# Kernel tuning notes

Hardware: AMD Instinct MI355X
Metric: run time of the kernel (lower is better)

The kernel has to match this reference:

```python
import jax, jax.numpy as jnp
import numpy as np

B, L, T = 32, 100, 50
V_SENT, V_FIELD, V_POS = 20000, 1500, 31
E_S, E_F, E_P = 400, 50, 5
FREP = E_F + 2 * E_P            # field rep = field + ppos + pneg embeds
H_DEC = 500                      # decoder hidden
H_DIR = H_DEC // 2               # per-direction encoder hidden
H_ENC = 500                      # encoder_hidden_size (attention/output dim)
IN_ENC = E_S + FREP
EPS = 1e-3


def lstm_cell(x, h, c, Wih, Whh, b):
    z = x @ Wih.T + h @ Whh.T + b
    i, f, g, o = jnp.split(z, 4, axis=-1)
    c = jax.nn.sigmoid(f) * c + jax.nn.sigmoid(i) * jnp.tanh(g)
    h = jax.nn.sigmoid(o) * jnp.tanh(c)
    return h, c


def setup_inputs():
    key = jax.random.key(0)
    ks = jax.random.split(key, 30)
    n = lambda k, sh, s=0.05: jax.random.normal(k, sh, jnp.float32) * s
    return {
        "value_mask": jnp.ones((B, L), jnp.float32),
        "align_prob": jax.random.uniform(ks[0], (B, L, V_SENT), jnp.float32),
        "E_sent": n(ks[1], (V_SENT, E_S)),
        "E_field": n(ks[2], (V_FIELD, E_F)),
        "E_ppos": n(ks[3], (V_POS, E_P)),
        "E_pneg": n(ks[4], (V_POS, E_P)),
        "E_target": n(ks[5], (V_SENT, 300)),
        "enc_Wih_f": n(ks[6], (4 * H_DIR, IN_ENC)),
        "enc_Whh_f": n(ks[7], (4 * H_DIR, H_DIR)),
        "enc_b_f": jnp.zeros((4 * H_DIR,), jnp.float32),
        "enc_Wih_b": n(ks[8], (4 * H_DIR, IN_ENC)),
        "enc_Whh_b": n(ks[9], (4 * H_DIR, H_DIR)),
        "enc_b_b": jnp.zeros((4 * H_DIR,), jnp.float32),
        "dec_Wih": n(ks[10], (4 * H_DEC, E_S)),
        "dec_Whh": n(ks[11], (4 * H_DEC, H_DEC)),
        "dec_b": jnp.zeros((4 * H_DEC,), jnp.float32),
        "W_d": n(ks[12], (H_DEC, H_ENC)),
        "W_z": n(ks[13], (H_DEC, FREP)),
        "W_out": n(ks[14], (H_DEC + H_ENC, H_ENC)),
        "b_out": jnp.zeros((H_ENC,), jnp.float32),
        "w_l": n(ks[15], (H_DEC + H_ENC + E_S, 1)),
        "b_l": jnp.zeros((1,), jnp.float32),
        "W_lin": n(ks[16], (V_SENT, H_ENC)),
        "b_lin": jnp.zeros((V_SENT,), jnp.float32),
        "sent": jax.random.randint(ks[17], (B, T), 0, V_SENT),
        "value": jax.random.randint(ks[18], (B, L), 0, V_SENT),
        "field": jax.random.randint(ks[19], (B, L), 0, V_FIELD),
        "ppos": jax.random.randint(ks[20], (B, L), 0, V_POS),
        "pneg": jax.random.randint(ks[21], (B, L), 0, V_POS),
        "batch_size": B,
    }


def _forward(value_mask, align_prob, E_sent, E_field, E_ppos, E_pneg, E_target,
             enc_Wih_f, enc_Whh_f, enc_b_f, enc_Wih_b, enc_Whh_b, enc_b_b,
             dec_Wih, dec_Whh, dec_b, W_d, W_z, W_out, b_out, w_l, b_l,
             W_lin, b_lin, sent, value, field, ppos, pneg):
    bsz = value.shape[0]
    inp_d = E_sent[value]                                             # [B,L,E_S]
    inp_z = jnp.concatenate([E_field[field], E_ppos[ppos], E_pneg[pneg]], axis=-1)  # [B,L,FREP]
    x = jnp.concatenate([inp_d, inp_z], axis=-1)                      # [B,L,IN_ENC]
    xs = jnp.transpose(x, (1, 0, 2))                                  # [L,B,IN_ENC]
    h0 = jnp.zeros((bsz, H_DIR), x.dtype)

    def enc_step(Wih, Whh, b):
        def f(carry, xt):
            h, c = lstm_cell(xt, carry[0], carry[1], Wih, Whh, b)
            return (h, c), h
        return f

    (hf, cf), hs_f = jax.lax.scan(enc_step(enc_Wih_f, enc_Whh_f, enc_b_f), (h0, h0), xs)
    (hb, cb), hs_b = jax.lax.scan(enc_step(enc_Wih_b, enc_Whh_b, enc_b_b), (h0, h0), xs[::-1])
    enc_out = jnp.transpose(jnp.concatenate([hs_f, hs_b[::-1]], axis=-1), (1, 0, 2))  # [B,L,H_ENC]
    # replicate torch .view on h_n [2,B,H_DIR] -> [B, 2*H_DIR] (row-major, as in source)
    h0_dec = jnp.stack([hf, hb]).reshape(bsz, 2 * H_DIR)
    c0_dec = jnp.stack([cf, cb]).reshape(bsz, 2 * H_DIR)

    sent_emb = jnp.transpose(E_sent[sent], (1, 0, 2))                 # [T,B,E_S]

    def dec_step(carry, xt):
        h, c = lstm_cell(xt, carry[0], carry[1], dec_Wih, dec_Whh, dec_b)
        s_d = jnp.einsum('be,ble->bl', h @ W_d, enc_out)              # attn over encoder states
        s_z = jnp.einsum('bf,blf->bl', h @ W_z, inp_z)                # attn over field reps
        a = jax.nn.softmax(s_d, axis=-1) * jax.nn.softmax(s_z, axis=-1)
        a = a / (jnp.sum(a, axis=-1, keepdims=True) + EPS)            # dual attention
        ctx = jnp.einsum('bl,ble->be', a, enc_out)
        hc = jnp.concatenate([h, ctx], axis=-1)
        out_t = jnp.tanh(hc @ W_out + b_out)                          # [B,H_ENC]
        lam_t = jax.nn.sigmoid(jnp.concatenate([hc, xt], axis=-1) @ w_l + b_l)  # [B,1]
        return (h, c), (out_t, a, lam_t)

    (hT, cT), (outs, attn, lam) = jax.lax.scan(dec_step, (h0_dec, c0_dec), sent_emb)
    outs = jnp.transpose(outs, (1, 0, 2))                             # [B,T,H_ENC]
    attn = jnp.transpose(attn, (1, 0, 2))                             # [B,T,L]
    lam = jnp.transpose(lam, (1, 0, 2))                               # [B,T,1]

    p_mod = jax.nn.log_softmax(outs @ W_lin.T + b_lin, axis=-1)       # [B,T,V]
    p_lex = jnp.einsum('btl,blv->btv', attn, align_prob)              # copy/lexical dist
    p_bias = jax.nn.log_softmax(lam * p_lex + (1.0 - lam) * p_mod, axis=-1)

    # vectorized replacement of the python double-loop position_idx_to_value
    max_idx = jnp.argmax(attn, axis=-1)                               # [B,T]
    word_idx = jnp.take_along_axis(value, max_idx, axis=1)            # [B,T]
    attn_pred = E_target[word_idx]                                    # [B,T,300]
    decoder_pred = E_target[jnp.argmax(p_bias, axis=-1)]              # [B,T,300]
    return p_bias, (hT, cT), attn_pred, decoder_pred


def reference(value_mask, align_prob, E_sent, E_field, E_ppos, E_pneg, E_target,
              enc_Wih_f, enc_Whh_f, enc_b_f, enc_Wih_b, enc_Whh_b, enc_b_b,
              dec_Wih, dec_Whh, dec_b, W_d, W_z, W_out, b_out, w_l, b_l,
              W_lin, b_lin, sent, value, field, ppos, pneg, batch_size):
    return _forward(value_mask, align_prob, E_sent, E_field, E_ppos, E_pneg, E_target,
                    enc_Wih_f, enc_Whh_f, enc_b_f, enc_Wih_b, enc_Whh_b, enc_b_b,
                    dec_Wih, dec_Whh, dec_b, W_d, W_z, W_out, b_out, w_l, b_l,
                    W_lin, b_lin, sent, value, field, ppos, pneg)
```

## Files before the change

### kernel.cpp

```cpp
#include <hip/hip_runtime.h>

#define DI __device__ __forceinline__

constexpr int B = 32, L = 100, T = 50;
constexpr int VS = 20000;
constexpr int HR = 250, HD = 500;
constexpr int INE = 460;
constexpr int OC = 1072;

constexpr size_t O_X      = 0;
constexpr size_t O_SX     = 5888000;
constexpr size_t O_WIHFT  = 8448000;
constexpr size_t O_WIHBT  = 10288000;
constexpr size_t O_WDECT  = 12128000;
constexpr size_t O_W4ENC  = 15328000;
constexpr size_t O_W4DEC  = 17328000;
constexpr size_t O_WCAT   = 21328000;
constexpr size_t O_XWF    = 23472000;
constexpr size_t O_XWB    = 49072000;
constexpr size_t O_XWD    = 74672000;
constexpr size_t O_EOB    = 100272000;
constexpr size_t O_E2     = 113072000;
constexpr size_t O_PROJ   = 125872000;
constexpr size_t O_EPZ    = O_PROJ;
constexpr size_t O_EHB    = O_PROJ + 2048000;
constexpr size_t O_DPZ    = O_PROJ + 2200000;
constexpr size_t O_DHB    = O_PROJ + 6300000;
constexpr size_t O_HD     = 139593600;
constexpr size_t O_H0DEC  = 146249600;
constexpr size_t O_HENCF  = 146505600;
constexpr size_t O_CENCF  = 146633600;
constexpr size_t O_CDEC0  = 146761600;
constexpr size_t O_HDECF  = 146889600;
constexpr size_t O_CDECF  = 147017600;
constexpr size_t O_AD     = 147145600;
constexpr size_t O_ATTN   = 148425600;
constexpr size_t O_EWL    = 149065600;
constexpr size_t O_SXL    = 149091200;
constexpr size_t O_AWL    = 149104000;
constexpr size_t O_LAM    = 149116800;
constexpr size_t O_LS1    = 149123200;
constexpr size_t O_WIDX   = 149129600;
constexpr size_t O_OUTS   = 149144192;
constexpr size_t O_FLG    = 154090496;

constexpr size_t OUT_HT  = 32000000;
constexpr size_t OUT_CT  = 32016000;
constexpr size_t OUT_AP  = 32032000;
constexpr size_t OUT_DP  = 32512000;

DI double dsig(double x) { return 1.0 / (1.0 + exp(-x)); }

DI double cld(const double* p) {
    return __hip_atomic_load(p, __ATOMIC_RELAXED, __HIP_MEMORY_SCOPE_AGENT);
}
DI void cst(double* p, double v) {
    __hip_atomic_store(p, v, __ATOMIC_RELAXED, __HIP_MEMORY_SCOPE_AGENT);
}
DI int cldi(const int* p) {
    return __hip_atomic_load(p, __ATOMIC_RELAXED, __HIP_MEMORY_SCOPE_AGENT);
}
DI void csti(int* p, int v) {
    __hip_atomic_store(p, v, __ATOMIC_RELAXED, __HIP_MEMORY_SCOPE_AGENT);
}
DI void spinge(const int* p, int target) {
    int spins = 0;
    while (cldi(p) < target) {
        __builtin_amdgcn_s_sleep(1);
        if (++spins > 50000000) break;
    }
}


__global__ void k_embed_x(const float* Es, const float* Ef, const float* Ep, const float* En,
                          const int* value, const int* field, const int* ppos, const int* pneg,
                          float* x) {
    int i = blockIdx.x * 256 + threadIdx.x;
    if (i >= B * L * INE) return;
    int j = i % INE, bl = i / INE;
    float v;
    if (j < 400)      v = Es[(size_t)value[bl] * 400 + j];
    else if (j < 450) v = Ef[(size_t)field[bl] * 50 + (j - 400)];
    else if (j < 455) v = Ep[(size_t)ppos[bl] * 5 + (j - 450)];
    else              v = En[(size_t)pneg[bl] * 5 + (j - 455)];
    x[i] = v;
}

__global__ void k_embed_sent(const float* Es, const int* sent, float* sx) {
    int i = blockIdx.x * 256 + threadIdx.x;
    if (i >= T * B * 400) return;
    int k = i % 400, tb = i / 400;
    int b = tb % B, t = tb / B;
    sx[i] = Es[(size_t)sent[b * T + t] * 400 + k];
}

__global__ void k_transpose(float* dst, const float* src, int K, int G) {
    int i = blockIdx.x * 256 + threadIdx.x;
    if (i >= K * G) return;
    int g = i % G, k = i / G;
    dst[i] = src[(size_t)g * K + k];
}

__global__ void k_pack4T(float* dst, const float* src, int U, int Kh) {
    int i = blockIdx.x * 256 + threadIdx.x;
    if (i >= U * Kh * 4) return;
    int g = i & 3, rest = i >> 2;
    int u = rest % U, k = rest / U;
    dst[i] = src[((size_t)(g * U + u)) * Kh + k];
}

__global__ void k_pack_wcat(float* dst, const float* Wd, const float* Wz, const float* Wo, const float* wl) {
    int i = blockIdx.x * 256 + threadIdx.x;
    if (i >= 500 * OC) return;
    int o = i % OC, d = i / OC;
    float v = 0.f;
    if (o < 500)       v = Wd[(size_t)d * 500 + o];
    else if (o < 560)  v = Wz[(size_t)d * 60 + (o - 500)];
    else if (o < 1060) v = Wo[(size_t)d * 500 + (o - 560)];
    else if (o == 1060) v = wl[d];
    dst[i] = v;
}

__global__ void k_zeroi(int* p, int n) {
    int i = blockIdx.x * 256 + threadIdx.x;
    if (i < n) p[i] = 0;
}

__global__ __launch_bounds__(256) void k_gemm_xw(double* out, const float* xs, int bstride, int tstride,
                                                 const float* Wt, const float* bias, int K, int G) {
    __shared__ float xls[460 * 33];
    int t = blockIdx.x;
    int g = blockIdx.y * 256 + threadIdx.x;
    bool act = g < G;
    for (int i = threadIdx.x; i < 32 * K; i += 256) {
        int b = i / K, k = i - b * K;
        xls[k * 33 + b] = xs[(size_t)b * bstride + (size_t)t * tstride + k];
    }
    __syncthreads();
    double acc[32];
    double bs = act ? (double)bias[g] : 0.0;
#pragma unroll
    for (int b = 0; b < 32; ++b) acc[b] = bs;
    for (int k = 0; k < K; ++k) {
        double w = act ? (double)Wt[(size_t)k * G + g] : 0.0;
        const float* xr = &xls[k * 33];
#pragma unroll
        for (int b = 0; b < 32; ++b) acc[b] += w * (double)xr[b];
    }
    if (act) {
#pragma unroll
        for (int b = 0; b < 32; ++b)
            out[((size_t)t * 32 + b) * G + g] = acc[b];
    }
}


__global__ __launch_bounds__(1024) void k_enc_split(const double* xw2F, const double* xw2B,
                                                    const float* w4T, double* PZ, double* HB,
                                                    int* FLG, double* eoB,
                                                    double* hencF, double* cencF) {
    __shared__ double h_s[256];
    __shared__ double pzL[3][250][4];
    int gid = blockIdx.x;
    int chain = gid >> 2, q = gid & 3;
    int dir = chain >> 5, b = chain & 31;
    int tid = threadIdx.x;
    int kc = tid >> 8, uu = tid & 255;
    bool act = uu < 250;
    int kq0 = (q * 250) >> 2, kq1 = ((q + 1) * 250) >> 2;
    int span = kq1 - kq0;
    int ks = kq0 + (span * kc) / 4, ke = kq0 + (span * (kc + 1)) / 4;
    int uq0 = kq0, uq1 = kq1;
    const double* xw = dir ? xw2B : xw2F;
    const float4* W = (const float4*)w4T + (size_t)dir * 250 * 250;
    double* myPZ = PZ + (size_t)(chain * 4 + q) * 1000;
    double* chPZ = PZ + (size_t)chain * 4000;
    double* myHB = HB + (size_t)chain * 256;
    int* flgA = FLG + chain * 128;
    int* flgB = flgA + 64;
    double c = 0.0;
    if (tid < 256) h_s[tid] = 0.0;
    __syncthreads();
    for (int s = 0; s < L; ++s) {
        int tin = dir ? (L - 1 - s) : s;
        double zi = 0.0, zf = 0.0, zg = 0.0, zo = 0.0;
        if (act) {
#pragma unroll 8
            for (int k = ks; k < ke; ++k) {
                float4 w = W[(size_t)k * 250 + uu];
                double hv = h_s[k];
                zi += (double)w.x * hv; zf += (double)w.y * hv;
                zg += (double)w.z * hv; zo += (double)w.w * hv;
            }
            if (kc) { pzL[kc - 1][uu][0] = zi; pzL[kc - 1][uu][1] = zf;
                      pzL[kc - 1][uu][2] = zg; pzL[kc - 1][uu][3] = zo; }
        }
        __syncthreads();
        if (act && kc == 0) {
            zi += pzL[0][uu][0] + pzL[1][uu][0] + pzL[2][uu][0];
            zf += pzL[0][uu][1] + pzL[1][uu][1] + pzL[2][uu][1];
            zg += pzL[0][uu][2] + pzL[1][uu][2] + pzL[2][uu][2];
            zo += pzL[0][uu][3] + pzL[1][uu][3] + pzL[2][uu][3];
            cst(&myPZ[uu * 4 + 0], zi); cst(&myPZ[uu * 4 + 1], zf);
            cst(&myPZ[uu * 4 + 2], zg); cst(&myPZ[uu * 4 + 3], zo);
        }
        __syncthreads();
        if (tid == 0) csti(&flgA[q * 16], s + 1);
        if (tid < 4) spinge(&flgA[tid * 16], s + 1);
        __syncthreads();
        if (kc == 0 && uu >= uq0 && uu < uq1) {
            const double* x0 = xw + ((size_t)tin * 32 + b) * 1000;
            double Zi = x0[0 * HR + uu], Zf = x0[1 * HR + uu];
            double Zg = x0[2 * HR + uu], Zo = x0[3 * HR + uu];
#pragma unroll
            for (int p = 0; p < 4; ++p) {
                if (p == q) { Zi += zi; Zf += zf; Zg += zg; Zo += zo; }
                else {
                    const double* pp = &chPZ[(size_t)p * 1000 + uu * 4];
                    Zi += cld(&pp[0]); Zf += cld(&pp[1]);
                    Zg += cld(&pp[2]); Zo += cld(&pp[3]);
                }
            }
            double cn = dsig(Zf) * c + dsig(Zi) * tanh(Zg);
            double hn = dsig(Zo) * tanh(cn);
            c = cn;
            cst(&myHB[uu], hn);
            eoB[((size_t)b * 100 + tin) * 500 + dir * 250 + uu] = hn;
            if (s == L - 1) {
                hencF[dir * 8000 + uu * 32 + b] = hn;
                cencF[dir * 8000 + uu * 32 + b] = cn;
            }
        }
        __syncthreads();
        if (tid == 0) csti(&flgB[q * 16], s + 1);
        if (tid < 4) spinge(&flgB[tid * 16], s + 1);
        __syncthreads();
        if (tid < 250) h_s[tid] = cld(&myHB[tid]);
        __syncthreads();
    }
}

__global__ void k_scramble(double* h0dec, double* cdec0, const double* hencF, const double* cencF) {
    int gt = blockIdx.x * 256 + threadIdx.x;
    if (gt >= 16000) return;
    int bb = gt / 500, j = gt - bb * 500;
    int d = gt / 8000, rem = gt - d * 8000;
    int bs = rem / 250, us = rem - bs * 250;
    h0dec[j * 32 + bb] = hencF[d * 8000 + us * 32 + bs];
    cdec0[j * 32 + bb] = cencF[d * 8000 + us * 32 + bs];
}


__global__ __launch_bounds__(1024) void k_dec_split8(const double* h0dec, const double* cdec0,
                                                     const double* xw2D, const float* w4T,
                                                     double* PZ, double* HB, int* FLG,
                                                     double* Hd, double* hdecF, double* cdecF) {
    __shared__ double h_s[512];
    __shared__ double pzL[500][4];
    int gid = blockIdx.x;
    int chain = gid >> 3, q = gid & 7;
    int b = chain;
    int tid = threadIdx.x;
    int kc = tid >> 9, uu = tid & 511;
    bool act = uu < 500;
    int kq0 = (q * 500) >> 3, kq1 = ((q + 1) * 500) >> 3;
    int span = kq1 - kq0;
    int ks = kq0 + (span * kc) / 2, ke = kq0 + (span * (kc + 1)) / 2;
    int uq0 = kq0, uq1 = kq1;
    const float4* W = (const float4*)w4T;
    double* myPZ = PZ + (size_t)(chain * 8 + q) * 2000;
    double* chPZ = PZ + (size_t)chain * 16000;
    double* myHB = HB + (size_t)chain * 512;
    int* flgA = FLG + chain * 256;
    int* flgB = flgA + 128;
    double c = (kc == 0 && uu >= uq0 && uu < uq1) ? cdec0[uu * 32 + b] : 0.0;
    if (tid < 512) h_s[tid] = (tid < 500) ? h0dec[tid * 32 + b] : 0.0;
    __syncthreads();
    for (int t = 0; t < T; ++t) {
        double zi = 0.0, zf = 0.0, zg = 0.0, zo = 0.0;
        if (act) {
#pragma unroll 8
            for (int k = ks; k < ke; ++k) {
                float4 w = W[(size_t)k * 500 + uu];
                double hv = h_s[k];
                zi += (double)w.x * hv; zf += (double)w.y * hv;
                zg += (double)w.z * hv; zo += (double)w.w * hv;
            }
            if (kc) { pzL[uu][0] = zi; pzL[uu][1] = zf; pzL[uu][2] = zg; pzL[uu][3] = zo; }
        }
        __syncthreads();
        if (act && kc == 0) {
            zi += pzL[uu][0]; zf += pzL[uu][1]; zg += pzL[uu][2]; zo += pzL[uu][3];
            cst(&myPZ[uu * 4 + 0], zi); cst(&myPZ[uu * 4 + 1], zf);
            cst(&myPZ[uu * 4 + 2], zg); cst(&myPZ[uu * 4 + 3], zo);
        }
        __syncthreads();
        if (tid == 0) csti(&flgA[q * 16], t + 1);
        if (tid < 8) spinge(&flgA[tid * 16], t + 1);
        __syncthreads();
        if (kc == 0 && uu >= uq0 && uu < uq1) {
            const double* x0 = xw2D + ((size_t)t * 32 + b) * 2000;
            double Zi = x0[0 * HD + uu], Zf = x0[1 * HD + uu];
            double Zg = x0[2 * HD + uu], Zo = x0[3 * HD + uu];
#pragma unroll
            for (int p = 0; p < 8; ++p) {
                if (p == q) { Zi += zi; Zf += zf; Zg += zg; Zo += zo; }
                else {
                    const double* pp = &chPZ[(size_t)p * 2000 + uu * 4];
                    Zi += cld(&pp[0]); Zf += cld(&pp[1]);
                    Zg += cld(&pp[2]); Zo += cld(&pp[3]);
                }
            }
            double cn = dsig(Zf) * c + dsig(Zi) * tanh(Zg);
            double hn = dsig(Zo) * tanh(cn);
            c = cn;
            cst(&myHB[uu], hn);
            Hd[((size_t)t * 32 + b) * 500 + uu] = hn;
            if (t == T - 1) {
                hdecF[uu * 32 + b] = hn;
                cdecF[uu * 32 + b] = cn;
            }
        }
        __syncthreads();
        if (tid == 0) csti(&flgB[q * 16], t + 1);
        if (tid < 8) spinge(&flgB[tid * 16], t + 1);
        __syncthreads();
        if (tid < 500) h_s[tid] = cld(&myHB[tid]);
        __syncthreads();
    }
}


__global__ __launch_bounds__(256) void k_e2_tiled(const double* eoB, const float* Wo, double* E2) {
    __shared__ double rows[8000];
    int et = blockIdx.x, mt = blockIdx.y;
    int tid = threadIdx.x;
    size_t rbase = (size_t)mt * 16 * 500;
    for (int i = tid; i < 8000; i += 256) rows[i] = eoB[rbase + i];
    __syncthreads();
    int e = et * 256 + tid;
    if (e >= 500) return;
    double acc[16];
#pragma unroll
    for (int m = 0; m < 16; ++m) acc[m] = 0.0;
    for (int d = 0; d < 500; ++d) {
        double w = (double)Wo[(size_t)(500 + d) * 500 + e];
#pragma unroll
        for (int m = 0; m < 16; ++m) acc[m] += rows[m * 500 + d] * w;
    }
#pragma unroll
    for (int m = 0; m < 16; ++m) E2[rbase + (size_t)m * 500 + e] = acc[m];
}

__global__ void k_ewl(const double* eoB, const float* wl, double* E_wl) {
    int w = threadIdx.x >> 6, lane = threadIdx.x & 63;
    int r = blockIdx.x * 4 + w;
    if (r >= 3200) return;
    const double* eo = eoB + (size_t)r * 500;
    double p = 0.0;
    for (int j = lane; j < 500; j += 64) p += eo[j] * (double)wl[500 + j];
    for (int off = 32; off > 0; off >>= 1) p += __shfl_down(p, off);
    if (lane == 0) E_wl[r] = p;
}

__global__ void k_sxl(const float* sx, const float* wl, double* SXL) {
    int i = blockIdx.x * 256 + threadIdx.x;
    if (i >= 1600) return;
    double acc = 0.0;
    for (int k = 0; k < 400; ++k) acc += (double)sx[(size_t)i * 400 + k] * (double)wl[1000 + k];
    SXL[i] = acc;
}

__global__ __launch_bounds__(256) void k_proj_tiled(const double* Hd, const float* Wcat, double* PROJ) {
    __shared__ double rows[8000];
    int ot = blockIdx.x, mt = blockIdx.y;
    int tid = threadIdx.x;
    size_t rbase = (size_t)mt * 16 * 500;
    for (int i = tid; i < 8000; i += 256) rows[i] = Hd[rbase + i];
    __syncthreads();
    int o = ot * 256 + tid;
    if (o >= OC) return;
    double acc[16];
#pragma unroll
    for (int m = 0; m < 16; ++m) acc[m] = 0.0;
    for (int d = 0; d < 500; ++d) {
        double w = (double)Wcat[(size_t)d * OC + o];
#pragma unroll
        for (int m = 0; m < 16; ++m) acc[m] += rows[m * 500 + d] * w;
    }
#pragma unroll
    for (int m = 0; m < 16; ++m)
        PROJ[((size_t)(mt * 16 + m)) * OC + o] = acc[m];
}

__global__ __launch_bounds__(256) void k_attn_all(
        const double* PROJ, const double* eoB, const float* x, const double* E_wl, const int* value,
        float* attn_ws, double* AD, double* AWL, int* widx) {
    int bid = blockIdx.x;
    int t = bid >> 5, b = bid & 31;
    int tid = threadIdx.x;
    int m = b * T + t;
    __shared__ double hwd_s[500], hz_s[60], sd_s[100], sz_s[100], aL[100];
    __shared__ double red[256];
    __shared__ int ri[256];
    const double* pr = PROJ + (size_t)bid * OC;
    for (int k = tid; k < 500; k += 256) hwd_s[k] = pr[k];
    if (tid < 60) hz_s[tid] = pr[500 + tid];
    __syncthreads();
    int w = tid >> 6, lane = tid & 63;
    for (int l = w; l < 100; l += 4) {
        const double* er = eoB + ((size_t)b * 100 + l) * 500;
        double p = 0.0;
        for (int e = lane; e < 500; e += 64) p += hwd_s[e] * er[e];
        for (int off = 32; off > 0; off >>= 1) p += __shfl_down(p, off);
        if (lane == 0) sd_s[l] = p;
        const float* zr = x + ((size_t)b * 100 + l) * 460 + 400;
        double q = (lane < 60) ? hz_s[lane] * (double)zr[lane] : 0.0;
        for (int off = 32; off > 0; off >>= 1) q += __shfl_down(q, off);
        if (lane == 0) sz_s[l] = q;
    }
    __syncthreads();
    red[tid] = (tid < 100) ? sd_s[tid] : -1e300; __syncthreads();
    for (int o = 128; o > 0; o >>= 1) { if (tid < o) red[tid] = fmax(red[tid], red[tid + o]); __syncthreads(); }
    double md = red[0]; __syncthreads();
    red[tid] = (tid < 100) ? exp(sd_s[tid] - md) : 0.0; __syncthreads();
    for (int o = 128; o > 0; o >>= 1) { if (tid < o) red[tid] += red[tid + o]; __syncthreads(); }
    double Sd = red[0]; __syncthreads();
    red[tid] = (tid < 100) ? sz_s[tid] : -1e300; __syncthreads();
    for (int o = 128; o > 0; o >>= 1) { if (tid < o) red[tid] = fmax(red[tid], red[tid + o]); __syncthreads(); }
    double mz = red[0]; __syncthreads();
    red[tid] = (tid < 100) ? exp(sz_s[tid] - mz) : 0.0; __syncthreads();
    for (int o = 128; o > 0; o >>= 1) { if (tid < o) red[tid] += red[tid + o]; __syncthreads(); }
    double Sz = red[0]; __syncthreads();
    if (tid < 100) aL[tid] = (exp(sd_s[tid] - md) / Sd) * (exp(sz_s[tid] - mz) / Sz);
    __syncthreads();
    red[tid] = (tid < 100) ? aL[tid] : 0.0; __syncthreads();
    for (int o = 128; o > 0; o >>= 1) { if (tid < o) red[tid] += red[tid + o]; __syncthreads(); }
    double Sa = red[0]; __syncthreads();
    if (tid < 100) {
        double av = aL[tid] / (Sa + 1e-3);
        aL[tid] = av;
        attn_ws[(size_t)m * 100 + tid] = (float)av;
        AD[(size_t)m * 100 + tid] = av;
    }
    __syncthreads();
    red[tid] = (tid < 100) ? aL[tid] : -1e300;
    ri[tid]  = (tid < 100) ? tid : 0x7fffffff;
    __syncthreads();
    for (int o = 128; o > 0; o >>= 1) {
        if (tid < o) {
            if (red[tid + o] > red[tid] || (red[tid + o] == red[tid] && ri[tid + o] < ri[tid])) {
                red[tid] = red[tid + o]; ri[tid] = ri[tid + o];
            }
        }
        __syncthreads();
    }
    if (tid == 0) widx[m] = value[b * 100 + ri[0]];
    if (tid < 64) {
        double p = (tid < 100) ? aL[tid] * E_wl[b * 100 + tid] : 0.0;
        if (tid + 64 < 100) p += aL[tid + 64] * E_wl[b * 100 + tid + 64];
        for (int off = 32; off > 0; off >>= 1) p += __shfl_down(p, off);
        if (tid == 0) AWL[m] = p;
    }
}

__global__ __launch_bounds__(256) void k_outs(const double* PROJ, const double* AD, const double* E2,
                                              const double* AWL, const double* SXL,
                                              const float* b_out, const float* b_l,
                                              float* outs32, float* lam_ws) {
    __shared__ double ad_s[100];
    int m = blockIdx.x, tid = threadIdx.x;
    int b = m / T, t = m - b * T;
    if (tid < 100) ad_s[tid] = AD[(size_t)m * 100 + tid];
    __syncthreads();
    const double* pr = PROJ + ((size_t)t * 32 + b) * OC;
#pragma unroll 2
    for (int e = tid; e < 512; e += 256) {
        if (e < 500) {
            double acc = pr[560 + e] + (double)b_out[e];
            const double* e2 = E2 + (size_t)b * 50000 + e;
            for (int l = 0; l < 100; ++l) acc += ad_s[l] * e2[l * 500];
            outs32[(size_t)m * 512 + e] = (float)tanh(acc);
        } else {
            outs32[(size_t)m * 512 + e] = 0.f;
        }
    }
    if (tid == 0)
        lam_ws[m] = (float)dsig(pr[1060] + AWL[m] + SXL[t * 32 + b] + (double)b_l[0]);
}

__global__ void k_hTcT(float* out, const double* hdecF, const double* cdecF) {
    int i = blockIdx.x * 256 + threadIdx.x;
    if (i >= 16000) return;
    int b = i / 500, u = i - b * 500;
    out[OUT_HT + i] = (float)hdecF[u * 32 + b];
    out[OUT_CT + i] = (float)cdecF[u * 32 + b];
}


__global__ __launch_bounds__(256) void k_gemm_logits_f32(const float* outs32, const float* W_lin,
                                                         const float* b_lin, float* d_out) {
    __shared__ float As[16][132], Bs[16][132];
    int n0 = blockIdx.x * 128, m0 = blockIdx.y * 128;
    int tid = threadIdx.x;
    int ty = tid >> 4, tx = tid & 15;
    int lr = tid >> 1, lh = tid & 1;
    float acc[8][8];
#pragma unroll
    for (int i = 0; i < 8; ++i)
#pragma unroll
        for (int j = 0; j < 8; ++j) acc[i][j] = 0.f;

    for (int k0 = 0; k0 < 512; k0 += 16) {
        int k8 = k0 + lh * 8;
        float4 a0, a1;
        int mrow = m0 + lr;
        if (mrow < 1600) {
            a0 = *(const float4*)(outs32 + (size_t)mrow * 512 + k8);
            a1 = *(const float4*)(outs32 + (size_t)mrow * 512 + k8 + 4);
        } else {
            a0 = make_float4(0.f, 0.f, 0.f, 0.f); a1 = a0;
        }
        float4 b0 = make_float4(0.f, 0.f, 0.f, 0.f), b1 = b0;
        int nrow = n0 + lr;
        if (nrow < VS) {
            if (k8 < 500)     b0 = *(const float4*)(W_lin + (size_t)nrow * 500 + k8);
            if (k8 + 4 < 500) b1 = *(const float4*)(W_lin + (size_t)nrow * 500 + k8 + 4);
        }
        __syncthreads();
        As[lh * 8 + 0][lr] = a0.x; As[lh * 8 + 1][lr] = a0.y;
        As[lh * 8 + 2][lr] = a0.z; As[lh * 8 + 3][lr] = a0.w;
        As[lh * 8 + 4][lr] = a1.x; As[lh * 8 + 5][lr] = a1.y;
        As[lh * 8 + 6][lr] = a1.z; As[lh * 8 + 7][lr] = a1.w;
        Bs[lh * 8 + 0][lr] = b0.x; Bs[lh * 8 + 1][lr] = b0.y;
        Bs[lh * 8 + 2][lr] = b0.z; Bs[lh * 8 + 3][lr] = b0.w;
        Bs[lh * 8 + 4][lr] = b1.x; Bs[lh * 8 + 5][lr] = b1.y;
        Bs[lh * 8 + 6][lr] = b1.z; Bs[lh * 8 + 7][lr] = b1.w;
        __syncthreads();
#pragma unroll
        for (int kk = 0; kk < 16; ++kk) {
            float4 av0 = *(const float4*)&As[kk][ty * 8];
            float4 av1 = *(const float4*)&As[kk][ty * 8 + 4];
            float4 bv0 = *(const float4*)&Bs[kk][tx * 8];
            float4 bv1 = *(const float4*)&Bs[kk][tx * 8 + 4];
            float ar[8] = {av0.x, av0.y, av0.z, av0.w, av1.x, av1.y, av1.z, av1.w};
            float br[8] = {bv0.x, bv0.y, bv0.z, bv0.w, bv1.x, bv1.y, bv1.z, bv1.w};
#pragma unroll
            for (int i = 0; i < 8; ++i)
#pragma unroll
                for (int j = 0; j < 8; ++j) acc[i][j] += ar[i] * br[j];
        }
    }
#pragma unroll
    for (int j = 0; j < 8; ++j) {
        int n = n0 + tx * 8 + j;
        if (n < VS) {
            float bl = b_lin[n];
#pragma unroll
            for (int i = 0; i < 8; ++i) {
                int mm = m0 + ty * 8 + i;
                if (mm < 1600)
                    d_out[(size_t)mm * VS + n] = acc[i][j] + bl;
            }
        }
    }
}


__global__ void k_red1(const float* d_out, float* LS1) {
    int m = blockIdx.x, tid = threadIdx.x;
    const float* row = d_out + (size_t)m * VS;
    __shared__ float red[256];
    float lm = -3e38f;
    for (int v = tid; v < VS; v += 256) lm = fmaxf(lm, row[v]);
    red[tid] = lm; __syncthreads();
    for (int o = 128; o > 0; o >>= 1) { if (tid < o) red[tid] = fmaxf(red[tid], red[tid + o]); __syncthreads(); }
    float m1 = red[0]; __syncthreads();
    float ls = 0.f;
    for (int v = tid; v < VS; v += 256) ls += expf(row[v] - m1);
    red[tid] = ls; __syncthreads();
    for (int o = 128; o > 0; o >>= 1) { if (tid < o) red[tid] += red[tid + o]; __syncthreads(); }
    if (tid == 0) LS1[m] = m1 + logf(red[0]);
}

__global__ __launch_bounds__(256) void k_plexmix(float* d_out, const float* attn_ws, const float* align_prob,
                                                 const float* lam_ws, const float* LS1) {
    int b = blockIdx.y, v0 = blockIdx.x * 64, tid = threadIdx.x;
    __shared__ float attn_s[50 * 100];
    __shared__ float al[100 * 64];
    for (int i = tid; i < 5000; i += 256) attn_s[i] = attn_ws[(size_t)b * 5000 + i];
    for (int i = tid; i < 6400; i += 256) {
        int l = i >> 6, j = i & 63;
        int v = v0 + j;
        al[i] = (v < VS) ? align_prob[((size_t)b * 100 + l) * VS + v] : 0.f;
    }
    __syncthreads();
    for (int idx = tid; idx < 50 * 64; idx += 256) {
        int t = idx >> 6, j = idx & 63;
        int v = v0 + j;
        if (v < VS) {
            float acc = 0.f;
            for (int l = 0; l < 100; ++l) acc += attn_s[t * 100 + l] * al[l * 64 + j];
            int m = b * T + t;
            size_t p = (size_t)m * VS + v;
            float lamv = lam_ws[m];
            d_out[p] = lamv * acc + (1.f - lamv) * (d_out[p] - LS1[m]);
        }
    }
}

__global__ void k_final2(float* d_out, const float* E_target) {
    int m = blockIdx.x, tid = threadIdx.x;
    float* row = d_out + (size_t)m * VS;
    __shared__ float sm[256], ss[256], sbv[256];
    __shared__ int sbi[256];
    float rm = -3e38f, rs = 0.f, bv = -3e38f; int bi = 0;
    for (int v = tid; v < VS; v += 256) {
        float xv = row[v];
        if (xv > bv) { bv = xv; bi = v; }
        if (xv > rm) { rs = rs * expf(rm - xv) + 1.f; rm = xv; }
        else rs += expf(xv - rm);
    }
    sm[tid] = rm; ss[tid] = rs; sbv[tid] = bv; sbi[tid] = bi;
    __syncthreads();
    for (int o = 128; o > 0; o >>= 1) {
        if (tid < o) {
            float m1 = sm[tid], m2 = sm[tid + o];
            float M = fmaxf(m1, m2);
            ss[tid] = ss[tid] * expf(m1 - M) + ss[tid + o] * expf(m2 - M);
            sm[tid] = M;
            if (sbv[tid + o] > sbv[tid] || (sbv[tid + o] == sbv[tid] && sbi[tid + o] < sbi[tid])) {
                sbv[tid] = sbv[tid + o]; sbi[tid] = sbi[tid + o];
            }
        }
        __syncthreads();
    }
    float ls2 = sm[0] + logf(ss[0]);
    int amax = sbi[0];
    for (int v = tid; v < VS; v += 256) row[v] -= ls2;
    for (int j = tid; j < 300; j += 256)
        d_out[OUT_DP + (size_t)m * 300 + j] = E_target[(size_t)amax * 300 + j];
}

__global__ void k_attnpred2(const int* widx, const float* E_target, float* d_out) {
    int i = blockIdx.x * 256 + threadIdx.x;
    if (i >= 1600 * 300) return;
    int m = i / 300, j = i - m * 300;
    d_out[OUT_AP + i] = E_target[(size_t)widx[m] * 300 + j];
}


extern "C" void kernel_launch(void* const* d_in, const int* in_sizes, int n_in,
                              void* d_out_v, int out_size, void* d_ws, size_t ws_size,
                              hipStream_t stream) {
    const float* align_prob = (const float*)d_in[1];
    const float* E_sent     = (const float*)d_in[2];
    const float* E_field    = (const float*)d_in[3];
    const float* E_ppos     = (const float*)d_in[4];
    const float* E_pneg     = (const float*)d_in[5];
    const float* E_target   = (const float*)d_in[6];
    const float* enc_Wih_f  = (const float*)d_in[7];
    const float* enc_Whh_f  = (const float*)d_in[8];
    const float* enc_b_f    = (const float*)d_in[9];
    const float* enc_Wih_b  = (const float*)d_in[10];
    const float* enc_Whh_b  = (const float*)d_in[11];
    const float* enc_b_b    = (const float*)d_in[12];
    const float* dec_Wih    = (const float*)d_in[13];
    const float* dec_Whh    = (const float*)d_in[14];
    const float* dec_b      = (const float*)d_in[15];
    const float* W_d        = (const float*)d_in[16];
    const float* W_z        = (const float*)d_in[17];
    const float* W_out      = (const float*)d_in[18];
    const float* b_out      = (const float*)d_in[19];
    const float* w_l        = (const float*)d_in[20];
    const float* b_l        = (const float*)d_in[21];
    const float* W_lin      = (const float*)d_in[22];
    const float* b_lin      = (const float*)d_in[23];
    const int* sent  = (const int*)d_in[24];
    const int* value = (const int*)d_in[25];
    const int* field = (const int*)d_in[26];
    const int* ppos  = (const int*)d_in[27];
    const int* pneg  = (const int*)d_in[28];

    char* ws = (char*)d_ws;
    float*  x      = (float*)(ws + O_X);
    float*  sx     = (float*)(ws + O_SX);
    float*  WihfT  = (float*)(ws + O_WIHFT);
    float*  WihbT  = (float*)(ws + O_WIHBT);
    float*  WdecT  = (float*)(ws + O_WDECT);
    float*  w4encT = (float*)(ws + O_W4ENC);
    float*  w4decT = (float*)(ws + O_W4DEC);
    float*  Wcat   = (float*)(ws + O_WCAT);
    double* xwF    = (double*)(ws + O_XWF);
    double* xwB    = (double*)(ws + O_XWB);
    double* xwD    = (double*)(ws + O_XWD);
    double* eoB    = (double*)(ws + O_EOB);
    double* E2     = (double*)(ws + O_E2);
    double* PROJ   = (double*)(ws + O_PROJ);
    double* EPZ    = (double*)(ws + O_EPZ);
    double* EHB    = (double*)(ws + O_EHB);
    double* DPZ    = (double*)(ws + O_DPZ);
    double* DHB    = (double*)(ws + O_DHB);
    double* Hd     = (double*)(ws + O_HD);
    double* h0dec  = (double*)(ws + O_H0DEC);
    double* hencF  = (double*)(ws + O_HENCF);
    double* cencF  = (double*)(ws + O_CENCF);
    double* cdec0  = (double*)(ws + O_CDEC0);
    double* hdecF  = (double*)(ws + O_HDECF);
    double* cdecF  = (double*)(ws + O_CDECF);
    double* AD     = (double*)(ws + O_AD);
    float*  attn_ws= (float*)(ws + O_ATTN);
    double* E_wl   = (double*)(ws + O_EWL);
    double* SXL    = (double*)(ws + O_SXL);
    double* AWL    = (double*)(ws + O_AWL);
    float*  lam_ws = (float*)(ws + O_LAM);
    float*  LS1    = (float*)(ws + O_LS1);
    int*    widx   = (int*)(ws + O_WIDX);
    float*  outs32 = (float*)(ws + O_OUTS);
    int*    FLGE   = (int*)(ws + O_FLG);
    int*    FLGD   = (int*)(ws + O_FLG) + 8192;
    float* out = (float*)d_out_v;

    k_embed_x<<<(B * L * INE + 255) / 256, 256, 0, stream>>>(E_sent, E_field, E_ppos, E_pneg,
                                                             value, field, ppos, pneg, x);
    k_embed_sent<<<(T * B * 400 + 255) / 256, 256, 0, stream>>>(E_sent, sent, sx);
    k_transpose<<<(460 * 1000 + 255) / 256, 256, 0, stream>>>(WihfT, enc_Wih_f, 460, 1000);
    k_transpose<<<(460 * 1000 + 255) / 256, 256, 0, stream>>>(WihbT, enc_Wih_b, 460, 1000);
    k_transpose<<<(400 * 2000 + 255) / 256, 256, 0, stream>>>(WdecT, dec_Wih, 400, 2000);
    k_pack4T<<<(250 * 250 * 4 + 255) / 256, 256, 0, stream>>>(w4encT, enc_Whh_f, 250, 250);
    k_pack4T<<<(250 * 250 * 4 + 255) / 256, 256, 0, stream>>>(w4encT + 250000, enc_Whh_b, 250, 250);
    k_pack4T<<<(500 * 500 * 4 + 255) / 256, 256, 0, stream>>>(w4decT, dec_Whh, 500, 500);
    k_pack_wcat<<<(500 * OC + 255) / 256, 256, 0, stream>>>(Wcat, W_d, W_z, W_out, w_l);
    k_zeroi<<<(16384 + 255) / 256, 256, 0, stream>>>(FLGE, 16384);
    k_sxl<<<(1600 + 255) / 256, 256, 0, stream>>>(sx, w_l, SXL);
    {
        dim3 g1(100, 4); k_gemm_xw<<<g1, 256, 0, stream>>>(xwF, x, L * INE, INE, WihfT, enc_b_f, 460, 1000);
        dim3 g2(100, 4); k_gemm_xw<<<g2, 256, 0, stream>>>(xwB, x, L * INE, INE, WihbT, enc_b_b, 460, 1000);
        dim3 g3(50, 8);  k_gemm_xw<<<g3, 256, 0, stream>>>(xwD, sx, 400, B * 400, WdecT, dec_b, 400, 2000);
    }

    k_enc_split<<<256, 1024, 0, stream>>>(xwF, xwB, w4encT, EPZ, EHB, FLGE, eoB, hencF, cencF);
    k_scramble<<<63, 256, 0, stream>>>(h0dec, cdec0, hencF, cencF);
    {
        dim3 ge(2, 200); k_e2_tiled<<<ge, 256, 0, stream>>>(eoB, W_out, E2);
    }
    k_ewl<<<800, 256, 0, stream>>>(eoB, w_l, E_wl);

    k_dec_split8<<<256, 1024, 0, stream>>>(h0dec, cdec0, xwD, w4decT, DPZ, DHB, FLGD,
                                           Hd, hdecF, cdecF);
    k_hTcT<<<63, 256, 0, stream>>>(out, hdecF, cdecF);

    {
        dim3 gp(5, 100); k_proj_tiled<<<gp, 256, 0, stream>>>(Hd, Wcat, PROJ);
    }
    k_attn_all<<<1600, 256, 0, stream>>>(PROJ, eoB, x, E_wl, value, attn_ws, AD, AWL, widx);
    k_outs<<<1600, 256, 0, stream>>>(PROJ, AD, E2, AWL, SXL, b_out, b_l, outs32, lam_ws);

    {
        dim3 gg(157, 13);
        k_gemm_logits_f32<<<gg, 256, 0, stream>>>(outs32, W_lin, b_lin, out);
    }
    k_red1<<<1600, 256, 0, stream>>>(out, LS1);
    {
        dim3 gp2(313, 32);
        k_plexmix<<<gp2, 256, 0, stream>>>(out, attn_ws, align_prob, lam_ws, LS1);
    }
    k_final2<<<1600, 256, 0, stream>>>(out, E_target);
    k_attnpred2<<<(1600 * 300 + 255) / 256, 256, 0, stream>>>(widx, E_target, out);
}
```

Baseline: 3.497 ms.

## Partition LSTM recurrence by hidden unit to remove one grid barrier per step

```diff
diff --git a/kernel.cpp b/kernel.cpp
--- a/kernel.cpp
+++ b/kernel.cpp
@@ -22,10 +22,8 @@
 constexpr size_t O_EOB    = 100272000;
 constexpr size_t O_E2     = 113072000;
 constexpr size_t O_PROJ   = 125872000;
-constexpr size_t O_EPZ    = O_PROJ;
-constexpr size_t O_EHB    = O_PROJ + 2048000;
-constexpr size_t O_DPZ    = O_PROJ + 2200000;
-constexpr size_t O_DHB    = O_PROJ + 6300000;
+constexpr size_t O_EHB    = O_PROJ;
+constexpr size_t O_DHB    = O_PROJ + 131072;
 constexpr size_t O_HD     = 139593600;
 constexpr size_t O_H0DEC  = 146249600;
 constexpr size_t O_HENCF  = 146505600;
@@ -155,29 +153,25 @@
 }
 
 
-__global__ __launch_bounds__(1024) void k_enc_split(const double* xw2F, const double* xw2B,
-                                                    const float* w4T, double* PZ, double* HB,
-                                                    int* FLG, double* eoB,
-                                                    double* hencF, double* cencF) {
+__global__ __launch_bounds__(1024) void k_enc_u(const double* xw2F, const double* xw2B,
+                                                const float* w4T, double* HB, int* FLG,
+                                                double* eoB, double* hencF, double* cencF) {
     __shared__ double h_s[256];
-    __shared__ double pzL[3][250][4];
+    __shared__ double pz[15][64][4];
     int gid = blockIdx.x;
     int chain = gid >> 2, q = gid & 3;
     int dir = chain >> 5, b = chain & 31;
     int tid = threadIdx.x;
-    int kc = tid >> 8, uu = tid & 255;
-    bool act = uu < 250;
-    int kq0 = (q * 250) >> 2, kq1 = ((q + 1) * 250) >> 2;
-    int span = kq1 - kq0;
-    int ks = kq0 + (span * kc) / 4, ke = kq0 + (span * (kc + 1)) / 4;
-    int uq0 = kq0, uq1 = kq1;
+    int kc = tid >> 6, ul = tid & 63;
+    int u0 = (q * 250) >> 2, u1 = ((q + 1) * 250) >> 2;
+    int nu = u1 - u0;
+    int u = u0 + ul;
+    bool act = ul < nu;
+    int ks = (kc * 250) >> 4, ke = ((kc + 1) * 250) >> 4;
     const double* xw = dir ? xw2B : xw2F;
     const float4* W = (const float4*)w4T + (size_t)dir * 250 * 250;
-    double* myPZ = PZ + (size_t)(chain * 4 + q) * 1000;
-    double* chPZ = PZ + (size_t)chain * 4000;
     double* myHB = HB + (size_t)chain * 256;
-    int* flgA = FLG + chain * 128;
-    int* flgB = flgA + 64;
+    int* flg = FLG + chain * 64;
     double c = 0.0;
     if (tid < 256) h_s[tid] = 0.0;
     __syncthreads();
@@ -185,55 +179,39 @@
         int tin = dir ? (L - 1 - s) : s;
         double zi = 0.0, zf = 0.0, zg = 0.0, zo = 0.0;
         if (act) {
-#pragma unroll 8
+#pragma unroll 4
             for (int k = ks; k < ke; ++k) {
-                float4 w = W[(size_t)k * 250 + uu];
+                float4 w = W[(size_t)k * 250 + u];
                 double hv = h_s[k];
                 zi += (double)w.x * hv; zf += (double)w.y * hv;
                 zg += (double)w.z * hv; zo += (double)w.w * hv;
             }
-            if (kc) { pzL[kc - 1][uu][0] = zi; pzL[kc - 1][uu][1] = zf;
-                      pzL[kc - 1][uu][2] = zg; pzL[kc - 1][uu][3] = zo; }
+            if (kc) { pz[kc - 1][ul][0] = zi; pz[kc - 1][ul][1] = zf;
+                      pz[kc - 1][ul][2] = zg; pz[kc - 1][ul][3] = zo; }
         }
         __syncthreads();
         if (act && kc == 0) {
-            zi += pzL[0][uu][0] + pzL[1][uu][0] + pzL[2][uu][0];
-            zf += pzL[0][uu][1] + pzL[1][uu][1] + pzL[2][uu][1];
-            zg += pzL[0][uu][2] + pzL[1][uu][2] + pzL[2][uu][2];
-            zo += pzL[0][uu][3] + pzL[1][uu][3] + pzL[2][uu][3];
-            cst(&myPZ[uu * 4 + 0], zi); cst(&myPZ[uu * 4 + 1], zf);
-            cst(&myPZ[uu * 4 + 2], zg); cst(&myPZ[uu * 4 + 3], zo);
-        }
-        __syncthreads();
-        if (tid == 0) csti(&flgA[q * 16], s + 1);
-        if (tid < 4) spinge(&flgA[tid * 16], s + 1);
-        __syncthreads();
-        if (kc == 0 && uu >= uq0 && uu < uq1) {
             const double* x0 = xw + ((size_t)tin * 32 + b) * 1000;
-            double Zi = x0[0 * HR + uu], Zf = x0[1 * HR + uu];
-            double Zg = x0[2 * HR + uu], Zo = x0[3 * HR + uu];
-#pragma unroll
-            for (int p = 0; p < 4; ++p) {
-                if (p == q) { Zi += zi; Zf += zf; Zg += zg; Zo += zo; }
-                else {
-                    const double* pp = &chPZ[(size_t)p * 1000 + uu * 4];
-                    Zi += cld(&pp[0]); Zf += cld(&pp[1]);
-                    Zg += cld(&pp[2]); Zo += cld(&pp[3]);
-                }
+            double Zi = x0[0 * HR + u] + zi, Zf = x0[1 * HR + u] + zf;
+            double Zg = x0[2 * HR + u] + zg, Zo = x0[3 * HR + u] + zo;
+#pragma unroll
+            for (int j = 0; j < 15; ++j) {
+                Zi += pz[j][ul][0]; Zf += pz[j][ul][1];
+                Zg += pz[j][ul][2]; Zo += pz[j][ul][3];
             }
             double cn = dsig(Zf) * c + dsig(Zi) * tanh(Zg);
             double hn = dsig(Zo) * tanh(cn);
             c = cn;
-            cst(&myHB[uu], hn);
-            eoB[((size_t)b * 100 + tin) * 500 + dir * 250 + uu] = hn;
+            cst(&myHB[u], hn);
+            eoB[((size_t)b * 100 + tin) * 500 + dir * 250 + u] = hn;
             if (s == L - 1) {
-                hencF[dir * 8000 + uu * 32 + b] = hn;
-                cencF[dir * 8000 + uu * 32 + b] = cn;
-            }
-        }
-        __syncthreads();
-        if (tid == 0) csti(&flgB[q * 16], s + 1);
-        if (tid < 4) spinge(&flgB[tid * 16], s + 1);
+                hencF[dir * 8000 + u * 32 + b] = hn;
+                cencF[dir * 8000 + u * 32 + b] = cn;
+            }
+        }
+        __syncthreads();
+        if (tid == 0) csti(&flg[q * 16], s + 1);
+        if (tid < 4) spinge(&flg[tid * 16], s + 1);
         __syncthreads();
         if (tid < 250) h_s[tid] = cld(&myHB[tid]);
         __syncthreads();
@@ -251,79 +229,64 @@
 }
 
 
-__global__ __launch_bounds__(1024) void k_dec_split8(const double* h0dec, const double* cdec0,
-                                                     const double* xw2D, const float* w4T,
-                                                     double* PZ, double* HB, int* FLG,
-                                                     double* Hd, double* hdecF, double* cdecF) {
+__global__ __launch_bounds__(1024) void k_dec_u(const double* h0dec, const double* cdec0,
+                                                const double* xw2D, const float* w4T,
+                                                double* HB, int* FLG,
+                                                double* Hd, double* hdecF, double* cdecF) {
     __shared__ double h_s[512];
-    __shared__ double pzL[500][4];
+    __shared__ double pz[15][64][4];
     int gid = blockIdx.x;
     int chain = gid >> 3, q = gid & 7;
     int b = chain;
     int tid = threadIdx.x;
-    int kc = tid >> 9, uu = tid & 511;
-    bool act = uu < 500;
-    int kq0 = (q * 500) >> 3, kq1 = ((q + 1) * 500) >> 3;
-    int span = kq1 - kq0;
-    int ks = kq0 + (span * kc) / 2, ke = kq0 + (span * (kc + 1)) / 2;
-    int uq0 = kq0, uq1 = kq1;
+    int kc = tid >> 6, ul = tid & 63;
+    int u0 = (q * 500) >> 3, u1 = ((q + 1) * 500) >> 3;
+    int nu = u1 - u0;
+    int u = u0 + ul;
+    bool act = ul < nu;
+    int ks = (kc * 500) >> 4, ke = ((kc + 1) * 500) >> 4;
     const float4* W = (const float4*)w4T;
-    double* myPZ = PZ + (size_t)(chain * 8 + q) * 2000;
-    double* chPZ = PZ + (size_t)chain * 16000;
     double* myHB = HB + (size_t)chain * 512;
-    int* flgA = FLG + chain * 256;
-    int* flgB = flgA + 128;
-    double c = (kc == 0 && uu >= uq0 && uu < uq1) ? cdec0[uu * 32 + b] : 0.0;
+    int* flg = FLG + chain * 128;
+    double c = (act && kc == 0) ? cdec0[u * 32 + b] : 0.0;
     if (tid < 512) h_s[tid] = (tid < 500) ? h0dec[tid * 32 + b] : 0.0;
     __syncthreads();
     for (int t = 0; t < T; ++t) {
         double zi = 0.0, zf = 0.0, zg = 0.0, zo = 0.0;
         if (act) {
-#pragma unroll 8
+#pragma unroll 4
             for (int k = ks; k < ke; ++k) {
-                float4 w = W[(size_t)k * 500 + uu];
+                float4 w = W[(size_t)k * 500 + u];
                 double hv = h_s[k];
                 zi += (double)w.x * hv; zf += (double)w.y * hv;
                 zg += (double)w.z * hv; zo += (double)w.w * hv;
             }
-            if (kc) { pzL[uu][0] = zi; pzL[uu][1] = zf; pzL[uu][2] = zg; pzL[uu][3] = zo; }
+            if (kc) { pz[kc - 1][ul][0] = zi; pz[kc - 1][ul][1] = zf;
+                      pz[kc - 1][ul][2] = zg; pz[kc - 1][ul][3] = zo; }
         }
         __syncthreads();
         if (act && kc == 0) {
-            zi += pzL[uu][0]; zf += pzL[uu][1]; zg += pzL[uu][2]; zo += pzL[uu][3];
-            cst(&myPZ[uu * 4 + 0], zi); cst(&myPZ[uu * 4 + 1], zf);
-            cst(&myPZ[uu * 4 + 2], zg); cst(&myPZ[uu * 4 + 3], zo);
-        }
-        __syncthreads();
-        if (tid == 0) csti(&flgA[q * 16], t + 1);
-        if (tid < 8) spinge(&flgA[tid * 16], t + 1);
-        __syncthreads();
-        if (kc == 0 && uu >= uq0 && uu < uq1) {
             const double* x0 = xw2D + ((size_t)t * 32 + b) * 2000;
-            double Zi = x0[0 * HD + uu], Zf = x0[1 * HD + uu];
-            double Zg = x0[2 * HD + uu], Zo = x0[3 * HD + uu];
-#pragma unroll
-            for (int p = 0; p < 8; ++p) {
-                if (p == q) { Zi += zi; Zf += zf; Zg += zg; Zo += zo; }
-                else {
-                    const double* pp = &chPZ[(size_t)p * 2000 + uu * 4];
-                    Zi += cld(&pp[0]); Zf += cld(&pp[1]);
-                    Zg += cld(&pp[2]); Zo += cld(&pp[3]);
-                }
+            double Zi = x0[0 * HD + u] + zi, Zf = x0[1 * HD + u] + zf;
+            double Zg = x0[2 * HD + u] + zg, Zo = x0[3 * HD + u] + zo;
+#pragma unroll
+            for (int j = 0; j < 15; ++j) {
+                Zi += pz[j][ul][0]; Zf += pz[j][ul][1];
+                Zg += pz[j][ul][2]; Zo += pz[j][ul][3];
             }
             double cn = dsig(Zf) * c + dsig(Zi) * tanh(Zg);
             double hn = dsig(Zo) * tanh(cn);
             c = cn;
-            cst(&myHB[uu], hn);
-            Hd[((size_t)t * 32 + b) * 500 + uu] = hn;
+            cst(&myHB[u], hn);
+            Hd[((size_t)t * 32 + b) * 500 + u] = hn;
             if (t == T - 1) {
-                hdecF[uu * 32 + b] = hn;
-                cdecF[uu * 32 + b] = cn;
-            }
-        }
-        __syncthreads();
-        if (tid == 0) csti(&flgB[q * 16], t + 1);
-        if (tid < 8) spinge(&flgB[tid * 16], t + 1);
+                hdecF[u * 32 + b] = hn;
+                cdecF[u * 32 + b] = cn;
+            }
+        }
+        __syncthreads();
+        if (tid == 0) csti(&flg[q * 16], t + 1);
+        if (tid < 8) spinge(&flg[tid * 16], t + 1);
         __syncthreads();
         if (tid < 500) h_s[tid] = cld(&myHB[tid]);
         __syncthreads();
@@ -697,9 +660,7 @@
     double* eoB    = (double*)(ws + O_EOB);
     double* E2     = (double*)(ws + O_E2);
     double* PROJ   = (double*)(ws + O_PROJ);
-    double* EPZ    = (double*)(ws + O_EPZ);
     double* EHB    = (double*)(ws + O_EHB);
-    double* DPZ    = (double*)(ws + O_DPZ);
     double* DHB    = (double*)(ws + O_DHB);
     double* Hd     = (double*)(ws + O_HD);
     double* h0dec  = (double*)(ws + O_H0DEC);
@@ -739,15 +700,14 @@
         dim3 g3(50, 8);  k_gemm_xw<<<g3, 256, 0, stream>>>(xwD, sx, 400, B * 400, WdecT, dec_b, 400, 2000);
     }
 
-    k_enc_split<<<256, 1024, 0, stream>>>(xwF, xwB, w4encT, EPZ, EHB, FLGE, eoB, hencF, cencF);
+    k_enc_u<<<256, 1024, 0, stream>>>(xwF, xwB, w4encT, EHB, FLGE, eoB, hencF, cencF);
     k_scramble<<<63, 256, 0, stream>>>(h0dec, cdec0, hencF, cencF);
     {
         dim3 ge(2, 200); k_e2_tiled<<<ge, 256, 0, stream>>>(eoB, W_out, E2);
     }
     k_ewl<<<800, 256, 0, stream>>>(eoB, w_l, E_wl);
 
-    k_dec_split8<<<256, 1024, 0, stream>>>(h0dec, cdec0, xwD, w4decT, DPZ, DHB, FLGD,
-                                           Hd, hdecF, cdecF);
+    k_dec_u<<<256, 1024, 0, stream>>>(h0dec, cdec0, xwD, w4decT, DHB, FLGD, Hd, hdecF, cdecF);
     k_hTcT<<<63, 256, 0, stream>>>(out, hdecF, cdecF);
 
     {
```

After: 3.178 ms. 1.1x faster.
